# Optimization experiments

Measured on AMD Instinct MI355X. Metric: run time of the kernel, lower is better.

## Reference

```python
import jax, jax.numpy as jnp
import numpy as np

N, FIN, HID, OUT = 12288, 500, 64, 16


def setup_inputs() -> dict:
    key = jax.random.key(0)
    k0, k1, k2, k3 = jax.random.split(key, 4)
    x = jax.random.normal(k0, (N, FIN), dtype=jnp.float32)
    # dense non-negative adjacency (weighted graph / learned graph structure)
    adj = jax.random.uniform(k1, (N, N), dtype=jnp.float32)
    s1 = 1.0 / np.sqrt(FIN)
    s2 = 1.0 / np.sqrt(HID)
    W1 = jax.random.uniform(k2, (FIN, HID), minval=-s1, maxval=s1, dtype=jnp.float32)
    b1 = jnp.zeros((HID,), jnp.float32)
    W2 = jax.random.uniform(k3, (HID, OUT), minval=-s2, maxval=s2, dtype=jnp.float32)
    b2 = jnp.zeros((OUT,), jnp.float32)
    return {"x": x, "adj": adj, "W1": W1, "b1": b1, "W2": W2, "b2": b2}


def reference(x, adj, W1, b1, W2, b2):
    # Eval mode: adjacency dropout and feature dropout are identity.
    # to_sparse() + spmm(A, H) == dense A @ H mathematically.
    h = adj @ (x @ W1 + b1)      # GCN layer 1: linear transform then neighbor aggregation
    h = jax.nn.relu(h)
    out = adj @ (h @ W2 + b2)    # GCN layer 2 (output layer, no activation)
    return out
```

## Files before the change

kernel.cpp:

```cpp
#include <hip/hip_runtime.h>

#define KD 12288
#define FIN 500
#define KPAD 512
#define HID 64
#define NOUT 16

typedef __attribute__((ext_vector_type(8))) short bf16x8;
typedef __attribute__((ext_vector_type(4))) float f32x4;

__device__ __forceinline__ unsigned short f2bf(float f) {
  union { float f; unsigned int u; } v; v.f = f;
  unsigned int u = v.u;
  unsigned int r = (u + 0x7fffu + ((u >> 16) & 1u)) >> 16;
  return (unsigned short)r;
}

__device__ __forceinline__ unsigned long long pack4(float4 v) {
  unsigned int lo = (unsigned int)f2bf(v.x) | ((unsigned int)f2bf(v.y) << 16);
  unsigned int hi = (unsigned int)f2bf(v.z) | ((unsigned int)f2bf(v.w) << 16);
  return (unsigned long long)lo | ((unsigned long long)hi << 32);
}

__device__ __forceinline__ f32x4 mfma16(bf16x8 a, bf16x8 b, f32x4 c) {
  return __builtin_amdgcn_mfma_f32_16x16x32_bf16(a, b, c, 0, 0, 0);
}

__device__ __forceinline__ int a_slot(int hg, int r, int ibyte) {
  return (((hg << 4) + r) << 4 | ibyte) ^ ((hg & 7) << 4);
}

__global__ void k_setup(const float* __restrict__ W1, const float* __restrict__ W2,
                        unsigned short* __restrict__ W1T, unsigned short* __restrict__ W2T) {
  int flat = blockIdx.x * 256 + threadIdx.x;
  if (flat < HID * KPAD) {
    int c = flat >> 9, k = flat & (KPAD - 1);
    W1T[flat] = (k < FIN) ? f2bf(W1[k * HID + c]) : (unsigned short)0;
  } else {
    int f2 = flat - HID * KPAD;
    if (f2 < NOUT * HID) {
      int c = f2 >> 6, k = f2 & 63;
      W2T[f2] = f2bf(W2[k * NOUT + c]);
    }
  }
}

__global__ __launch_bounds__(256) void k_g1(const float* __restrict__ x,
                                            const unsigned short* __restrict__ W1T,
                                            const float* __restrict__ b1,
                                            unsigned short* __restrict__ h1T) {
  __shared__ unsigned char Ab[2][2048];
  __shared__ unsigned short tr[64][16];
  const int tid = threadIdx.x;
  const int w = tid >> 6, l = tid & 63;
  const int r0 = blockIdx.x << 4;
  const int sr = tid >> 4, sk4 = (tid & 15) << 2;
  const int shg = sk4 >> 3;
  const int aw = a_slot(shg, sr, (sk4 & 7) << 1);
  const int fr = l & 15, fg = l >> 4;
  const int ar0 = a_slot(fg, fr, 0);
  const int ar1 = a_slot(4 + fg, fr, 0);
  const float* ap = x + (size_t)(r0 + sr) * FIN;
  const unsigned short* bp = W1T + (w * 16 + fr) * KPAD + (fg << 3);
  f32x4 acc = {0.f, 0.f, 0.f, 0.f};
  for (int s = 0; s < KPAD / 64; ++s) {
    int k0 = s * 64 + sk4;
    float4 av = make_float4(0.f, 0.f, 0.f, 0.f);
    if (k0 < FIN) av = *(const float4*)(ap + k0);
    unsigned char* buf = Ab[s & 1];
    *(unsigned long long*)(buf + aw) = pack4(av);
    __syncthreads();
    bf16x8 a0 = *(const bf16x8*)(buf + ar0);
    bf16x8 a1 = *(const bf16x8*)(buf + ar1);
    bf16x8 b0 = *(const bf16x8*)(bp + s * 64);
    bf16x8 b1v = *(const bf16x8*)(bp + s * 64 + 32);
    acc = mfma16(a0, b0, acc);
    acc = mfma16(a1, b1v, acc);
    __syncthreads();
  }
  const int c = w * 16 + fr;
  const float bias = b1[c];
#pragma unroll
  for (int q = 0; q < 4; ++q) tr[c][fg * 4 + q] = f2bf(acc[q] + bias);
  __syncthreads();
  int cc = tid >> 2, rr = (tid & 3) << 2;
  *(unsigned long long*)(h1T + (size_t)cc * KD + r0 + rr) = *(unsigned long long*)&tr[cc][rr];
}

__global__ __launch_bounds__(256) void k_l1(const float* __restrict__ adj,
                                            const unsigned short* __restrict__ h1T,
                                            unsigned short* __restrict__ H) {
  __shared__ unsigned char Ab[2][2048];
  const int tid = threadIdx.x;
  const int w = tid >> 6, l = tid & 63;
  const int r0 = blockIdx.x << 4;
  const int sr = tid >> 4, sk4 = (tid & 15) << 2;
  const int shg = sk4 >> 3;
  const int aw = a_slot(shg, sr, (sk4 & 7) << 1);
  const int fr = l & 15, fg = l >> 4;
  const int ar0 = a_slot(fg, fr, 0);
  const int ar1 = a_slot(4 + fg, fr, 0);
  const float* ap = adj + (size_t)(r0 + sr) * KD + sk4;
  const unsigned short* bp = h1T + (size_t)(w * 16 + fr) * KD + (fg << 3);
  f32x4 acc = {0.f, 0.f, 0.f, 0.f};
  float4 av = *(const float4*)ap;
  bf16x8 bv0 = *(const bf16x8*)(bp);
  bf16x8 bv1 = *(const bf16x8*)(bp + 32);
#pragma unroll 2
  for (int s = 0; s < KD / 64; ++s) {
    unsigned char* buf = Ab[s & 1];
    *(unsigned long long*)(buf + aw) = pack4(av);
    int sn = (s < KD / 64 - 1) ? s + 1 : s;
    av = *(const float4*)(ap + (size_t)sn * 64);
    __syncthreads();
    bf16x8 a0 = *(const bf16x8*)(buf + ar0);
    bf16x8 a1 = *(const bf16x8*)(buf + ar1);
    bf16x8 nb0 = *(const bf16x8*)(bp + (size_t)sn * 64);
    bf16x8 nb1 = *(const bf16x8*)(bp + (size_t)sn * 64 + 32);
    acc = mfma16(a0, bv0, acc);
    acc = mfma16(a1, bv1, acc);
    bv0 = nb0; bv1 = nb1;
  }
  const int c = w * 16 + fr;
#pragma unroll
  for (int q = 0; q < 4; ++q) {
    float v = acc[q];
    v = v > 0.f ? v : 0.f;
    H[(size_t)(r0 + fg * 4 + q) * HID + c] = f2bf(v);
  }
}

__global__ __launch_bounds__(64) void k_g2(const unsigned short* __restrict__ Hm,
                                           const unsigned short* __restrict__ W2T,
                                           const float* __restrict__ b2,
                                           unsigned short* __restrict__ h2T) {
  __shared__ unsigned char Ab[2048];
  __shared__ unsigned short tr[16][16];
  const int l = threadIdx.x;
  const int r0 = blockIdx.x << 4;
  const int fr = l & 15, fg = l >> 4;
  const int sr = l >> 2;
#pragma unroll
  for (int j = 0; j < 4; ++j) {
    int k4 = (l & 3) * 16 + j * 4;
    int hg = k4 >> 3;
    unsigned long long v = *(const unsigned long long*)(Hm + (size_t)(r0 + sr) * HID + k4);
    *(unsigned long long*)(Ab + a_slot(hg, sr, (k4 & 7) << 1)) = v;
  }
  __syncthreads();
  bf16x8 a0 = *(const bf16x8*)(Ab + a_slot(fg, fr, 0));
  bf16x8 a1 = *(const bf16x8*)(Ab + a_slot(4 + fg, fr, 0));
  bf16x8 b0 = *(const bf16x8*)(W2T + fr * HID + fg * 8);
  bf16x8 b1v = *(const bf16x8*)(W2T + fr * HID + 32 + fg * 8);
  f32x4 acc = {0.f, 0.f, 0.f, 0.f};
  acc = mfma16(a0, b0, acc);
  acc = mfma16(a1, b1v, acc);
  const float bias = b2[fr];
#pragma unroll
  for (int q = 0; q < 4; ++q) tr[fr][fg * 4 + q] = f2bf(acc[q] + bias);
  __syncthreads();
  int cc = l >> 2, rr = (l & 3) << 2;
  *(unsigned long long*)(h2T + (size_t)cc * KD + r0 + rr) = *(unsigned long long*)&tr[cc][rr];
}

__global__ __launch_bounds__(256) void k_l2(const float* __restrict__ adj,
                                            const unsigned short* __restrict__ h2T,
                                            float* __restrict__ out) {
  __shared__ unsigned char Ab[4][2][2048];
  __shared__ float red[4][16][16];
  const int tid = threadIdx.x;
  const int w = tid >> 6, l = tid & 63;
  const int r0 = blockIdx.x << 4;
  const int kb = w * (KD / 4);
  const int fr = l & 15, fg = l >> 4;
  const int sr = l >> 4, sk4 = (l & 15) << 2;
  const int shg = sk4 >> 3;
  const int ar0 = a_slot(fg, fr, 0);
  const int ar1 = a_slot(4 + fg, fr, 0);
  const float* ap0 = adj + (size_t)(r0 + sr) * KD + kb + sk4;
  const unsigned short* bp = h2T + (size_t)fr * KD + kb + (fg << 3);
  f32x4 acc = {0.f, 0.f, 0.f, 0.f};
  float4 av[4];
#pragma unroll
  for (int j = 0; j < 4; ++j) av[j] = *(const float4*)(ap0 + (size_t)(4 * j) * KD);
  bf16x8 bv0 = *(const bf16x8*)(bp);
  bf16x8 bv1 = *(const bf16x8*)(bp + 32);
  const int NS = (KD / 4) / 64;
  for (int s = 0; s < NS; ++s) {
    unsigned char* buf = Ab[w][s & 1];
#pragma unroll
    for (int j = 0; j < 4; ++j) {
      int row = sr + 4 * j;
      *(unsigned long long*)(buf + a_slot(shg, row, (sk4 & 7) << 1)) = pack4(av[j]);
    }
    int sn = (s < NS - 1) ? s + 1 : s;
#pragma unroll
    for (int j = 0; j < 4; ++j) av[j] = *(const float4*)(ap0 + (size_t)(4 * j) * KD + sn * 64);
    bf16x8 a0 = *(const bf16x8*)(buf + ar0);
    bf16x8 a1 = *(const bf16x8*)(buf + ar1);
    bf16x8 nb0 = *(const bf16x8*)(bp + sn * 64);
    bf16x8 nb1 = *(const bf16x8*)(bp + sn * 64 + 32);
    acc = mfma16(a0, bv0, acc);
    acc = mfma16(a1, bv1, acc);
    bv0 = nb0; bv1 = nb1;
  }
#pragma unroll
  for (int q = 0; q < 4; ++q) red[w][fg * 4 + q][fr] = acc[q];
  __syncthreads();
  int rr = tid >> 4, cc = tid & 15;
  float sum = red[0][rr][cc] + red[1][rr][cc] + red[2][rr][cc] + red[3][rr][cc];
  out[(size_t)(r0 + rr) * NOUT + cc] = sum;
}

extern "C" void kernel_launch(void* const* d_in, const int* in_sizes, int n_in,
                              void* d_out, int out_size, void* d_ws, size_t ws_size,
                              hipStream_t stream) {
  const float* x   = (const float*)d_in[0];
  const float* adj = (const float*)d_in[1];
  const float* W1  = (const float*)d_in[2];
  const float* b1  = (const float*)d_in[3];
  const float* W2  = (const float*)d_in[4];
  const float* b2  = (const float*)d_in[5];
  float* out = (float*)d_out;
  char* ws = (char*)d_ws;
  unsigned short* W1T = (unsigned short*)(ws);
  unsigned short* W2T = (unsigned short*)(ws + 65536);
  unsigned short* h1T = (unsigned short*)(ws + 67584);
  unsigned short* Hm  = (unsigned short*)(ws + 1640448);
  unsigned short* h2T = (unsigned short*)(ws + 3213312);

  hipLaunchKernelGGL(k_setup, dim3(132), dim3(256), 0, stream, W1, W2, W1T, W2T);
  hipLaunchKernelGGL(k_g1, dim3(KD / 16), dim3(256), 0, stream, x, W1T, b1, h1T);
  hipLaunchKernelGGL(k_l1, dim3(KD / 16), dim3(256), 0, stream, adj, h1T, Hm);
  hipLaunchKernelGGL(k_g2, dim3(KD / 16), dim3(64), 0, stream, Hm, W2T, b2, h2T);
  hipLaunchKernelGGL(k_l2, dim3(KD / 16), dim3(256), 0, stream, adj, h2T, out);
}
```

Measured before the change: 960.6 us.

## Load adjacency directly into MFMA fragments, drop LDS staging, double-buffer registers

Both aggregation kernels now have each lane load its own A-fragment of the fp32 adjacency straight from global memory and convert it to bf16 in registers. This removes the LDS write/read round trip and, in k_l1, the per-step __syncthreads. Loads are software-pipelined two steps ahead using A/B register sets. The catch: each wave in k_l1 now loads the full 16-row adjacency tile redundantly (four waves share the same rows), and access is less coalesced per lane. This relies on cache hits and adds register pressure.

```diff
diff --git a/kernel.cpp b/kernel.cpp
--- a/kernel.cpp
+++ b/kernel.cpp
@@ -20,6 +20,12 @@
   unsigned int lo = (unsigned int)f2bf(v.x) | ((unsigned int)f2bf(v.y) << 16);
   unsigned int hi = (unsigned int)f2bf(v.z) | ((unsigned int)f2bf(v.w) << 16);
   return (unsigned long long)lo | ((unsigned long long)hi << 32);
+}
+
+__device__ __forceinline__ bf16x8 cvt8(float4 lo, float4 hi) {
+  union { unsigned long long u[2]; bf16x8 v; } r;
+  r.u[0] = pack4(lo); r.u[1] = pack4(hi);
+  return r.v;
 }
 
 __device__ __forceinline__ f32x4 mfma16(bf16x8 a, bf16x8 b, f32x4 c) {
@@ -90,36 +96,49 @@
 __global__ __launch_bounds__(256) void k_l1(const float* __restrict__ adj,
                                             const unsigned short* __restrict__ h1T,
                                             unsigned short* __restrict__ H) {
-  __shared__ unsigned char Ab[2][2048];
   const int tid = threadIdx.x;
   const int w = tid >> 6, l = tid & 63;
   const int r0 = blockIdx.x << 4;
-  const int sr = tid >> 4, sk4 = (tid & 15) << 2;
-  const int shg = sk4 >> 3;
-  const int aw = a_slot(shg, sr, (sk4 & 7) << 1);
-  const int fr = l & 15, fg = l >> 4;
-  const int ar0 = a_slot(fg, fr, 0);
-  const int ar1 = a_slot(4 + fg, fr, 0);
-  const float* ap = adj + (size_t)(r0 + sr) * KD + sk4;
+  const int fr = l & 15, fg = l >> 4;
+  const float* ap = adj + (size_t)(r0 + fr) * KD + (fg << 3);
   const unsigned short* bp = h1T + (size_t)(w * 16 + fr) * KD + (fg << 3);
   f32x4 acc = {0.f, 0.f, 0.f, 0.f};
-  float4 av = *(const float4*)ap;
-  bf16x8 bv0 = *(const bf16x8*)(bp);
-  bf16x8 bv1 = *(const bf16x8*)(bp + 32);
-#pragma unroll 2
-  for (int s = 0; s < KD / 64; ++s) {
-    unsigned char* buf = Ab[s & 1];
-    *(unsigned long long*)(buf + aw) = pack4(av);
-    int sn = (s < KD / 64 - 1) ? s + 1 : s;
-    av = *(const float4*)(ap + (size_t)sn * 64);
-    __syncthreads();
-    bf16x8 a0 = *(const bf16x8*)(buf + ar0);
-    bf16x8 a1 = *(const bf16x8*)(buf + ar1);
-    bf16x8 nb0 = *(const bf16x8*)(bp + (size_t)sn * 64);
-    bf16x8 nb1 = *(const bf16x8*)(bp + (size_t)sn * 64 + 32);
-    acc = mfma16(a0, bv0, acc);
-    acc = mfma16(a1, bv1, acc);
-    bv0 = nb0; bv1 = nb1;
+  const int NS = KD / 64;
+  float4 aA0, aA1, aA2, aA3, aB0, aB1, aB2, aB3;
+  bf16x8 bA0, bA1, bB0, bB1;
+  {
+    const float* p = ap;
+    aA0 = *(const float4*)(p);      aA1 = *(const float4*)(p + 4);
+    aA2 = *(const float4*)(p + 32); aA3 = *(const float4*)(p + 36);
+    const unsigned short* q = bp;
+    bA0 = *(const bf16x8*)(q);      bA1 = *(const bf16x8*)(q + 32);
+    p = ap + 64;
+    aB0 = *(const float4*)(p);      aB1 = *(const float4*)(p + 4);
+    aB2 = *(const float4*)(p + 32); aB3 = *(const float4*)(p + 36);
+    q = bp + 64;
+    bB0 = *(const bf16x8*)(q);      bB1 = *(const bf16x8*)(q + 32);
+  }
+  for (int s = 0; s < NS; s += 2) {
+    acc = mfma16(cvt8(aA0, aA1), bA0, acc);
+    acc = mfma16(cvt8(aA2, aA3), bA1, acc);
+    {
+      int sn = (s + 2 < NS) ? s + 2 : s;
+      const float* p = ap + (size_t)sn * 64;
+      aA0 = *(const float4*)(p);      aA1 = *(const float4*)(p + 4);
+      aA2 = *(const float4*)(p + 32); aA3 = *(const float4*)(p + 36);
+      const unsigned short* q = bp + (size_t)sn * 64;
+      bA0 = *(const bf16x8*)(q);      bA1 = *(const bf16x8*)(q + 32);
+    }
+    acc = mfma16(cvt8(aB0, aB1), bB0, acc);
+    acc = mfma16(cvt8(aB2, aB3), bB1, acc);
+    {
+      int sn = (s + 3 < NS) ? s + 3 : s + 1;
+      const float* p = ap + (size_t)sn * 64;
+      aB0 = *(const float4*)(p);      aB1 = *(const float4*)(p + 4);
+      aB2 = *(const float4*)(p + 32); aB3 = *(const float4*)(p + 36);
+      const unsigned short* q = bp + (size_t)sn * 64;
+      bB0 = *(const bf16x8*)(q);      bB1 = *(const bf16x8*)(q + 32);
+    }
   }
   const int c = w * 16 + fr;
 #pragma unroll
@@ -166,43 +185,51 @@
 __global__ __launch_bounds__(256) void k_l2(const float* __restrict__ adj,
                                             const unsigned short* __restrict__ h2T,
                                             float* __restrict__ out) {
-  __shared__ unsigned char Ab[4][2][2048];
   __shared__ float red[4][16][16];
   const int tid = threadIdx.x;
   const int w = tid >> 6, l = tid & 63;
   const int r0 = blockIdx.x << 4;
   const int kb = w * (KD / 4);
   const int fr = l & 15, fg = l >> 4;
-  const int sr = l >> 4, sk4 = (l & 15) << 2;
-  const int shg = sk4 >> 3;
-  const int ar0 = a_slot(fg, fr, 0);
-  const int ar1 = a_slot(4 + fg, fr, 0);
-  const float* ap0 = adj + (size_t)(r0 + sr) * KD + kb + sk4;
+  const float* ap = adj + (size_t)(r0 + fr) * KD + kb + (fg << 3);
   const unsigned short* bp = h2T + (size_t)fr * KD + kb + (fg << 3);
   f32x4 acc = {0.f, 0.f, 0.f, 0.f};
-  float4 av[4];
-#pragma unroll
-  for (int j = 0; j < 4; ++j) av[j] = *(const float4*)(ap0 + (size_t)(4 * j) * KD);
-  bf16x8 bv0 = *(const bf16x8*)(bp);
-  bf16x8 bv1 = *(const bf16x8*)(bp + 32);
   const int NS = (KD / 4) / 64;
-  for (int s = 0; s < NS; ++s) {
-    unsigned char* buf = Ab[w][s & 1];
-#pragma unroll
-    for (int j = 0; j < 4; ++j) {
-      int row = sr + 4 * j;
-      *(unsigned long long*)(buf + a_slot(shg, row, (sk4 & 7) << 1)) = pack4(av[j]);
-    }
-    int sn = (s < NS - 1) ? s + 1 : s;
-#pragma unroll
-    for (int j = 0; j < 4; ++j) av[j] = *(const float4*)(ap0 + (size_t)(4 * j) * KD + sn * 64);
-    bf16x8 a0 = *(const bf16x8*)(buf + ar0);
-    bf16x8 a1 = *(const bf16x8*)(buf + ar1);
-    bf16x8 nb0 = *(const bf16x8*)(bp + sn * 64);
-    bf16x8 nb1 = *(const bf16x8*)(bp + sn * 64 + 32);
-    acc = mfma16(a0, bv0, acc);
-    acc = mfma16(a1, bv1, acc);
-    bv0 = nb0; bv1 = nb1;
+  float4 aA0, aA1, aA2, aA3, aB0, aB1, aB2, aB3;
+  bf16x8 bA0, bA1, bB0, bB1;
+  {
+    const float* p = ap;
+    aA0 = *(const float4*)(p);      aA1 = *(const float4*)(p + 4);
+    aA2 = *(const float4*)(p + 32); aA3 = *(const float4*)(p + 36);
+    const unsigned short* q = bp;
+    bA0 = *(const bf16x8*)(q);      bA1 = *(const bf16x8*)(q + 32);
+    p = ap + 64;
+    aB0 = *(const float4*)(p);      aB1 = *(const float4*)(p + 4);
+    aB2 = *(const float4*)(p + 32); aB3 = *(const float4*)(p + 36);
+    q = bp + 64;
+    bB0 = *(const bf16x8*)(q);      bB1 = *(const bf16x8*)(q + 32);
+  }
+  for (int s = 0; s < NS; s += 2) {
+    acc = mfma16(cvt8(aA0, aA1), bA0, acc);
+    acc = mfma16(cvt8(aA2, aA3), bA1, acc);
+    {
+      int sn = (s + 2 < NS) ? s + 2 : s;
+      const float* p = ap + (size_t)sn * 64;
+      aA0 = *(const float4*)(p);      aA1 = *(const float4*)(p + 4);
+      aA2 = *(const float4*)(p + 32); aA3 = *(const float4*)(p + 36);
+      const unsigned short* q = bp + (size_t)sn * 64;
+      bA0 = *(const bf16x8*)(q);      bA1 = *(const bf16x8*)(q + 32);
+    }
+    acc = mfma16(cvt8(aB0, aB1), bB0, acc);
+    acc = mfma16(cvt8(aB2, aB3), bB1, acc);
+    {
+      int sn = (s + 3 < NS) ? s + 3 : s + 1;
+      const float* p = ap + (size_t)sn * 64;
+      aB0 = *(const float4*)(p);      aB1 = *(const float4*)(p + 4);
+      aB2 = *(const float4*)(p + 32); aB3 = *(const float4*)(p + 36);
+      const unsigned short* q = bp + (size_t)sn * 64;
+      bB0 = *(const bf16x8*)(q);      bB1 = *(const bf16x8*)(q + 32);
+    }
   }
 #pragma unroll
   for (int q = 0; q < 4; ++q) red[w][fg * 4 + q][fr] = acc[q];
```

Measured after the change: 1.576 ms. +64.1%, slower.

## Use async global-to-LDS loads with 4-stage pipeline in adjacency GEMMs

Applied to the files above, without the earlier changes.

Both adjacency aggregation kernels now stream fp32 adj tiles and bf16 feature tiles directly into shared memory through global_load_lds, using a 4-deep ring buffer with XOR swizzling and vmcnt-based waits. The bf16 conversion moves to the LDS read side. The second layer is re-tiled to 64-row blocks with a 4-way K split, reduced via atomicAdd into an output that the setup kernel now zeroes. The aim is to hide HBM latency on the two 600MB adj reads and raise memory throughput. The cost is more LDS use, fp32 atomics that make the sum order nondeterministic, and one extra zeroing pass.

```diff
diff --git a/kernel.cpp b/kernel.cpp
--- a/kernel.cpp
+++ b/kernel.cpp
@@ -9,6 +9,15 @@
 typedef __attribute__((ext_vector_type(8))) short bf16x8;
 typedef __attribute__((ext_vector_type(4))) float f32x4;
 
+typedef __attribute__((address_space(1))) const unsigned int GU;
+typedef __attribute__((address_space(3))) unsigned int LU;
+
+__device__ __forceinline__ void gload16(const void* g, void* l) {
+  __builtin_amdgcn_global_load_lds((GU*)g, (LU*)l, 16, 0, 0);
+}
+#define WAITV(N) asm volatile("s_waitcnt vmcnt(" #N ")" ::: "memory")
+#define BAR() do { __builtin_amdgcn_s_barrier(); __builtin_amdgcn_sched_barrier(0); } while (0)
+
 __device__ __forceinline__ unsigned short f2bf(float f) {
   union { float f; unsigned int u; } v; v.f = f;
   unsigned int u = v.u;
@@ -22,6 +31,12 @@
   return (unsigned long long)lo | ((unsigned long long)hi << 32);
 }
 
+__device__ __forceinline__ bf16x8 cvt8(float4 lo, float4 hi) {
+  union { unsigned long long u[2]; bf16x8 v; } r;
+  r.u[0] = pack4(lo); r.u[1] = pack4(hi);
+  return r.v;
+}
+
 __device__ __forceinline__ f32x4 mfma16(bf16x8 a, bf16x8 b, f32x4 c) {
   return __builtin_amdgcn_mfma_f32_16x16x32_bf16(a, b, c, 0, 0, 0);
 }
@@ -31,17 +46,19 @@
 }
 
 __global__ void k_setup(const float* __restrict__ W1, const float* __restrict__ W2,
-                        unsigned short* __restrict__ W1T, unsigned short* __restrict__ W2T) {
+                        unsigned short* __restrict__ W1T, unsigned short* __restrict__ W2T,
+                        float* __restrict__ out) {
   int flat = blockIdx.x * 256 + threadIdx.x;
   if (flat < HID * KPAD) {
     int c = flat >> 9, k = flat & (KPAD - 1);
     W1T[flat] = (k < FIN) ? f2bf(W1[k * HID + c]) : (unsigned short)0;
+  } else if (flat < HID * KPAD + NOUT * HID) {
+    int f2 = flat - HID * KPAD;
+    int c = f2 >> 6, k = f2 & 63;
+    W2T[f2] = f2bf(W2[k * NOUT + c]);
   } else {
-    int f2 = flat - HID * KPAD;
-    if (f2 < NOUT * HID) {
-      int c = f2 >> 6, k = f2 & 63;
-      W2T[f2] = f2bf(W2[k * NOUT + c]);
-    }
+    int f3 = flat - (HID * KPAD + NOUT * HID);
+    if (f3 < KD * NOUT) out[f3] = 0.f;
   }
 }
 
@@ -90,37 +107,61 @@
 __global__ __launch_bounds__(256) void k_l1(const float* __restrict__ adj,
                                             const unsigned short* __restrict__ h1T,
                                             unsigned short* __restrict__ H) {
-  __shared__ unsigned char Ab[2][2048];
+  __shared__ __align__(1024) unsigned char As[4][4096];
+  __shared__ __align__(1024) unsigned char Bs[4][8192];
   const int tid = threadIdx.x;
   const int w = tid >> 6, l = tid & 63;
   const int r0 = blockIdx.x << 4;
-  const int sr = tid >> 4, sk4 = (tid & 15) << 2;
-  const int shg = sk4 >> 3;
-  const int aw = a_slot(shg, sr, (sk4 & 7) << 1);
-  const int fr = l & 15, fg = l >> 4;
-  const int ar0 = a_slot(fg, fr, 0);
-  const int ar1 = a_slot(4 + fg, fr, 0);
-  const float* ap = adj + (size_t)(r0 + sr) * KD + sk4;
-  const unsigned short* bp = h1T + (size_t)(w * 16 + fr) * KD + (fg << 3);
-  f32x4 acc = {0.f, 0.f, 0.f, 0.f};
-  float4 av = *(const float4*)ap;
-  bf16x8 bv0 = *(const bf16x8*)(bp);
-  bf16x8 bv1 = *(const bf16x8*)(bp + 32);
-#pragma unroll 2
-  for (int s = 0; s < KD / 64; ++s) {
-    unsigned char* buf = Ab[s & 1];
-    *(unsigned long long*)(buf + aw) = pack4(av);
-    int sn = (s < KD / 64 - 1) ? s + 1 : s;
-    av = *(const float4*)(ap + (size_t)sn * 64);
-    __syncthreads();
-    bf16x8 a0 = *(const bf16x8*)(buf + ar0);
-    bf16x8 a1 = *(const bf16x8*)(buf + ar1);
-    bf16x8 nb0 = *(const bf16x8*)(bp + (size_t)sn * 64);
-    bf16x8 nb1 = *(const bf16x8*)(bp + (size_t)sn * 64 + 32);
-    acc = mfma16(a0, bv0, acc);
-    acc = mfma16(a1, bv1, acc);
-    bv0 = nb0; bv1 = nb1;
-  }
+  const int fr = l & 15, fg = l >> 4;
+  const int sr = tid >> 4;
+  const int sc = (tid & 15) ^ (sr & 7);
+  const float* aRun = adj + (size_t)(r0 + sr) * KD + (sc << 2);
+  const int bc = tid >> 3;
+  const int bh = (tid & 7) ^ (bc & 7);
+  const unsigned short* bRun = h1T + (size_t)bc * KD + (bh << 3);
+  const unsigned char* aW = (const unsigned char*)&As[0][0] + (w << 10);
+  const unsigned char* bW = (const unsigned char*)&Bs[0][0] + (w << 10);
+  const int x7 = fr & 7;
+  const int aOff0 = fr * 256 + ((((fg << 1) | 0) ^ x7) << 4);
+  const int aOff1 = fr * 256 + ((((fg << 1) | 1) ^ x7) << 4);
+  const int aOff2 = fr * 256 + (((8 + (fg << 1)) ^ x7) << 4);
+  const int aOff3 = fr * 256 + (((9 + (fg << 1)) ^ x7) << 4);
+  const int cB = w * 16 + fr;
+  const int bOff0 = cB * 128 + ((fg ^ (cB & 7)) << 4);
+  const int bOff1 = cB * 128 + (((4 + fg) ^ (cB & 7)) << 4);
+  f32x4 acc = {0.f, 0.f, 0.f, 0.f};
+  const int NS = KD / 64;
+#pragma unroll
+  for (int d = 0; d < 3; ++d) {
+    gload16(aRun, (void*)(aW + d * 4096));
+    gload16(bRun, (void*)(bW + d * 8192));
+    gload16(bRun + (size_t)32 * KD, (void*)(bW + d * 8192 + 4096));
+    aRun += 64; bRun += 64;
+  }
+#define L1_COMPUTE(S)                                                          \
+  {                                                                            \
+    const unsigned char* ab = (const unsigned char*)&As[(S) & 3][0];           \
+    const unsigned char* bb = (const unsigned char*)&Bs[(S) & 3][0];           \
+    bf16x8 a0 = cvt8(*(const float4*)(ab + aOff0), *(const float4*)(ab + aOff1)); \
+    bf16x8 a1 = cvt8(*(const float4*)(ab + aOff2), *(const float4*)(ab + aOff3)); \
+    bf16x8 b0 = *(const bf16x8*)(bb + bOff0);                                  \
+    bf16x8 b1 = *(const bf16x8*)(bb + bOff1);                                  \
+    acc = mfma16(a0, b0, acc);                                                 \
+    acc = mfma16(a1, b1, acc);                                                 \
+  }
+  for (int s = 0; s < NS - 3; ++s) {
+    WAITV(6);
+    BAR();
+    int d = (s + 3) & 3;
+    gload16(aRun, (void*)(aW + d * 4096));
+    gload16(bRun, (void*)(bW + d * 8192));
+    gload16(bRun + (size_t)32 * KD, (void*)(bW + d * 8192 + 4096));
+    aRun += 64; bRun += 64;
+    L1_COMPUTE(s);
+  }
+  WAITV(6); BAR(); L1_COMPUTE(NS - 3);
+  WAITV(3); BAR(); L1_COMPUTE(NS - 2);
+  WAITV(0); BAR(); L1_COMPUTE(NS - 1);
   const int c = w * 16 + fr;
 #pragma unroll
   for (int q = 0; q < 4; ++q) {
@@ -166,50 +207,59 @@
 __global__ __launch_bounds__(256) void k_l2(const float* __restrict__ adj,
                                             const unsigned short* __restrict__ h2T,
                                             float* __restrict__ out) {
-  __shared__ unsigned char Ab[4][2][2048];
-  __shared__ float red[4][16][16];
+  __shared__ __align__(1024) unsigned char As[4][8192];
+  __shared__ __align__(1024) unsigned char Bs[4][1024];
   const int tid = threadIdx.x;
   const int w = tid >> 6, l = tid & 63;
-  const int r0 = blockIdx.x << 4;
-  const int kb = w * (KD / 4);
-  const int fr = l & 15, fg = l >> 4;
-  const int sr = l >> 4, sk4 = (l & 15) << 2;
-  const int shg = sk4 >> 3;
-  const int ar0 = a_slot(fg, fr, 0);
-  const int ar1 = a_slot(4 + fg, fr, 0);
-  const float* ap0 = adj + (size_t)(r0 + sr) * KD + kb + sk4;
-  const unsigned short* bp = h2T + (size_t)fr * KD + kb + (fg << 3);
-  f32x4 acc = {0.f, 0.f, 0.f, 0.f};
-  float4 av[4];
-#pragma unroll
-  for (int j = 0; j < 4; ++j) av[j] = *(const float4*)(ap0 + (size_t)(4 * j) * KD);
-  bf16x8 bv0 = *(const bf16x8*)(bp);
-  bf16x8 bv1 = *(const bf16x8*)(bp + 32);
-  const int NS = (KD / 4) / 64;
-  for (int s = 0; s < NS; ++s) {
-    unsigned char* buf = Ab[w][s & 1];
-#pragma unroll
-    for (int j = 0; j < 4; ++j) {
-      int row = sr + 4 * j;
-      *(unsigned long long*)(buf + a_slot(shg, row, (sk4 & 7) << 1)) = pack4(av[j]);
-    }
-    int sn = (s < NS - 1) ? s + 1 : s;
-#pragma unroll
-    for (int j = 0; j < 4; ++j) av[j] = *(const float4*)(ap0 + (size_t)(4 * j) * KD + sn * 64);
-    bf16x8 a0 = *(const bf16x8*)(buf + ar0);
-    bf16x8 a1 = *(const bf16x8*)(buf + ar1);
-    bf16x8 nb0 = *(const bf16x8*)(bp + sn * 64);
-    bf16x8 nb1 = *(const bf16x8*)(bp + sn * 64 + 32);
-    acc = mfma16(a0, bv0, acc);
-    acc = mfma16(a1, bv1, acc);
-    bv0 = nb0; bv1 = nb1;
-  }
-#pragma unroll
-  for (int q = 0; q < 4; ++q) red[w][fg * 4 + q][fr] = acc[q];
-  __syncthreads();
-  int rr = tid >> 4, cc = tid & 15;
-  float sum = red[0][rr][cc] + red[1][rr][cc] + red[2][rr][cc] + red[3][rr][cc];
-  out[(size_t)(r0 + rr) * NOUT + cc] = sum;
+  const int bt = blockIdx.x;
+  const int r0 = (bt >> 2) << 6;
+  const int kb = (bt & 3) * (KD / 4);
+  const int fr = l & 15, fg = l >> 4;
+  const int sR = tid >> 3;
+  const int sc = (tid & 7) ^ (sR & 7);
+  const float* aRun = adj + (size_t)(r0 + sR) * KD + kb + (sc << 2);
+  const int bc = l >> 2;
+  const int bh = (l & 3) ^ (bc & 3);
+  const unsigned short* bRun = h2T + (size_t)bc * KD + kb + (bh << 3);
+  const unsigned char* aW = (const unsigned char*)&As[0][0] + (w << 10);
+  const unsigned char* bW = (const unsigned char*)&Bs[0][0];
+  const int R = (w << 4) + fr;
+  const int aOff0 = R * 128 + ((((fg << 1) | 0) ^ (R & 7)) << 4);
+  const int aOff1 = R * 128 + ((((fg << 1) | 1) ^ (R & 7)) << 4);
+  const int bOff = fr * 64 + ((fg ^ (fr & 3)) << 4);
+  f32x4 acc = {0.f, 0.f, 0.f, 0.f};
+  const int NS = (KD / 4) / 32;
+#pragma unroll
+  for (int d = 0; d < 3; ++d) {
+    gload16(aRun, (void*)(aW + d * 8192));
+    gload16(aRun + (size_t)32 * KD, (void*)(aW + d * 8192 + 4096));
+    gload16(bRun, (void*)(bW + d * 1024));
+    aRun += 32; bRun += 32;
+  }
+#define L2_COMPUTE(S)                                                          \
+  {                                                                            \
+    const unsigned char* ab = (const unsigned char*)&As[(S) & 3][0];           \
+    const unsigned char* bb = (const unsigned char*)&Bs[(S) & 3][0];           \
+    bf16x8 a = cvt8(*(const float4*)(ab + aOff0), *(const float4*)(ab + aOff1)); \
+    bf16x8 b = *(const bf16x8*)(bb + bOff);                                    \
+    acc = mfma16(a, b, acc);                                                   \
+  }
+  for (int s = 0; s < NS - 3; ++s) {
+    WAITV(6);
+    BAR();
+    int d = (s + 3) & 3;
+    gload16(aRun, (void*)(aW + d * 8192));
+    gload16(aRun + (size_t)32 * KD, (void*)(aW + d * 8192 + 4096));
+    gload16(bRun, (void*)(bW + d * 1024));
+    aRun += 32; bRun += 32;
+    L2_COMPUTE(s);
+  }
+  WAITV(6); BAR(); L2_COMPUTE(NS - 3);
+  WAITV(3); BAR(); L2_COMPUTE(NS - 2);
+  WAITV(0); BAR(); L2_COMPUTE(NS - 1);
+  float* op = out + (size_t)(r0 + (w << 4) + (fg << 2)) * NOUT + fr;
+#pragma unroll
+  for (int q = 0; q < 4; ++q) atomicAdd(op + q * NOUT, acc[q]);
 }
 
 extern "C" void kernel_launch(void* const* d_in, const int* in_sizes, int n_in,
@@ -229,9 +279,9 @@
   unsigned short* Hm  = (unsigned short*)(ws + 1640448);
   unsigned short* h2T = (unsigned short*)(ws + 3213312);
 
-  hipLaunchKernelGGL(k_setup, dim3(132), dim3(256), 0, stream, W1, W2, W1T, W2T);
+  hipLaunchKernelGGL(k_setup, dim3(900), dim3(256), 0, stream, W1, W2, W1T, W2T, out);
   hipLaunchKernelGGL(k_g1, dim3(KD / 16), dim3(256), 0, stream, x, W1T, b1, h1T);
   hipLaunchKernelGGL(k_l1, dim3(KD / 16), dim3(256), 0, stream, adj, h1T, Hm);
   hipLaunchKernelGGL(k_g2, dim3(KD / 16), dim3(64), 0, stream, Hm, W2T, b2, h2T);
-  hipLaunchKernelGGL(k_l2, dim3(KD / 16), dim3(256), 0, stream, adj, h2T, out);
-}
+  hipLaunchKernelGGL(k_l2, dim3((KD / 64) * 4), dim3(256), 0, stream, adj, h2T, out);
+}
```

New measurement: 967.8 us. Within noise of the previous version (+0.8%).
